# Kernel optimization log

Measured on AMD Instinct MI355X. Metric: run time of the kernel, lower is better.

The kernel has to match this reference:

```python
import jax, jax.numpy as jnp
import numpy as np

N = 20000      # nodes
E = 320000     # edges
B = 128        # graphs in batch
DIN = 64       # in_channels == out_channels (residual)
DEDGE = 64     # edge_attr_dim
DINS = 64      # ins_dim
H = 2          # heads
C = 64         # out_channels per head
L = 2          # num_ins (conv layers)
SLOPE = 0.2    # leaky relu negative slope
EPS = 1e-5     # batchnorm eps


def setup_inputs() -> dict:
    key = jax.random.key(0)
    ks = jax.random.split(key, 12)
    s = 0.05  # small glorot-ish init scale
    return {
        "x": jax.random.normal(ks[0], (N, DIN), jnp.float32),
        "edge_index": jax.random.randint(ks[1], (2, E), 0, N),
        "edge_attr": jax.random.normal(ks[2], (E, DEDGE), jnp.float32),
        "instr_vectors": jax.random.normal(ks[3], (L, B, DINS), jnp.float32),
        "batch": jnp.sort(jax.random.randint(ks[4], (N,), 0, B)),
        "W_l": jax.random.normal(ks[5], (L, DIN + DINS, H * C), jnp.float32) * s,
        "W_e": jax.random.normal(ks[6], (L, DEDGE + DINS, H * C), jnp.float32) * s,
        "att_l": jax.random.normal(ks[7], (L, H, C), jnp.float32) * s,
        "att_r": jax.random.normal(ks[8], (L, H, C), jnp.float32) * s,
        "att_e": jax.random.normal(ks[9], (L, H, C), jnp.float32) * s,
        "bias": jnp.zeros((L, C), jnp.float32),
        "bn_gamma": jnp.ones((L - 1, C), jnp.float32),
        "bn_beta": jnp.zeros((L - 1, C), jnp.float32),
    }


def reference(x, edge_index, edge_attr, instr_vectors, batch,
              W_l, W_e, att_l, att_r, att_e, bias, bn_gamma, bn_beta):
    src, dst = edge_index[0], edge_index[1]  # j -> i (source_to_target)
    h = x
    for i in range(L):
        ins = instr_vectors[i]                                   # [B, DINS]
        x_cat = jnp.concatenate([h, ins[batch]], axis=-1)        # [N, DIN+DINS]
        e_cat = jnp.concatenate([edge_attr, ins[batch[src]]], axis=-1)  # [E, ...]
        xl = (x_cat @ W_l[i]).reshape(-1, H, C)                  # [N,H,C] (lin_l == lin_r)
        al = (xl * att_l[i]).sum(-1)                             # [N,H]
        ar = (xl * att_r[i]).sum(-1)                             # [N,H]
        eh = (e_cat @ W_e[i]).reshape(-1, H, C)                  # [E,H,C]
        ae = (eh * att_e[i]).sum(-1)                             # [E,H]
        a = al[src] + ar[dst] + ae                               # [E,H]
        a = jnp.where(a > 0, a, SLOPE * a)                       # leaky relu
        # segment softmax over incoming edges of each target node
        m = jax.ops.segment_max(a, dst, num_segments=N)          # [N,H]
        ex = jnp.exp(a - m[dst])
        ssum = jax.ops.segment_sum(ex, dst, num_segments=N)
        alpha = ex / (ssum[dst] + 1e-16)                         # [E,H]
        out = jax.ops.segment_sum(xl[src] * alpha[:, :, None], dst, num_segments=N)
        out = out.mean(axis=1) + bias[i]                         # concat=False -> head mean
        h = out + h                                              # residual
        if i != L - 1:
            mu = h.mean(axis=0)
            var = ((h - mu) ** 2).mean(axis=0)                   # biased var (BN training)
            h = (h - mu) / jnp.sqrt(var + EPS) * bn_gamma[i] + bn_beta[i]
            h = jax.nn.relu(h)
    return h
```

## Files before the change

### kernel.cpp

```cpp
#include <hip/hip_runtime.h>
#include <hip/hip_fp16.h>
#include <math.h>

#define NN 20000
#define NE 320000
#define NB 128
#define SLOPE 0.2f
#define BN_EPS 1e-5f
#define ROWS 65
#define PBKT 256

__device__ __forceinline__ unsigned short f2bf(float f) {
    unsigned int u = __float_as_uint(f);
    unsigned int r = (u + 0x7FFFu + ((u >> 16) & 1u)) >> 16;
    return (unsigned short)r;
}
__device__ __forceinline__ float bf2f(unsigned short h) {
    return __uint_as_float(((unsigned int)h) << 16);
}

__global__ __launch_bounds__(256) void k_front(const int* __restrict__ dst, int* __restrict__ deg,
                                               const float* __restrict__ instr, const float* __restrict__ Wl,
                                               const float* __restrict__ We, const float* __restrict__ atte,
                                               float* __restrict__ insl01, float* __restrict__ ve01,
                                               float* __restrict__ ce01) {
    __shared__ float w2[128];
    int blk = blockIdx.x, t = threadIdx.x;
    if (blk < 1250) {
        int e = blk * 256 + t;
        atomicAdd(&deg[dst[e]], 1);
    } else if (blk < 1378) {
        int bb = blk - 1250;
        int L = bb >> 6;
        int idx = (bb & 63) * 256 + t;
        int b = idx >> 7, j = idx & 127;
        const float* ins = instr + (size_t)L * NB * 64;
        const float* WlL = Wl + (size_t)L * 128 * 128;
        float acc = 0.f;
        for (int k = 0; k < 64; ++k) acc += ins[b * 64 + k] * WlL[(64 + k) * 128 + j];
        insl01[(size_t)L * 16384 + idx] = acc;
    } else {
        int L = blk - 1378;
        const float* WeL = We + (size_t)L * 128 * 128;
        const float* aeL = atte + L * 128;
        int h = (t >> 6) & 1;
        int k = t & 63;
        int row = (t < 128) ? k : (64 + k);
        float acc = 0.f;
        for (int c = 0; c < 64; ++c) acc += WeL[row * 128 + h * 64 + c] * aeL[h * 64 + c];
        if (t < 128) ve01[L * 128 + t] = acc;
        else        w2[t - 128] = acc;
        __syncthreads();
        int b = t >> 1, hh = t & 1;
        const float* ins = instr + (size_t)L * NB * 64;
        float a2 = 0.f;
        for (int kk = 0; kk < 64; ++kk) a2 += ins[b * 64 + kk] * w2[hh * 64 + kk];
        ce01[L * 256 + b * 2 + hh] = a2;
    }
}

__global__ __launch_bounds__(1024) void k_scan(const int* __restrict__ deg,
                                               int* __restrict__ rowptr, int* __restrict__ cursor) {
    __shared__ int wsum[16];
    int t = threadIdx.x, lane = t & 63, w = t >> 6;
    int running = 0;
    for (int r = 0; r < 20; ++r) {
        int idx = r * 1024 + t;
        int v = (idx < NN) ? deg[idx] : 0;
        int incl = v;
        for (int off = 1; off < 64; off <<= 1) { int u = __shfl_up(incl, off); if (lane >= off) incl += u; }
        if (lane == 63) wsum[w] = incl;
        __syncthreads();
        int pre = 0, tot = 0;
        for (int i = 0; i < 16; ++i) { int s = wsum[i]; tot += s; if (i < w) pre += s; }
        int excl = running + pre + incl - v;
        if (idx < NN) { rowptr[idx] = excl; cursor[idx] = excl; }
        running += tot;
        __syncthreads();
    }
    if (t == 0) rowptr[NN] = running;
}

__global__ __launch_bounds__(256) void k_node(const float* __restrict__ hcur, const float* __restrict__ Wl,
                                              const float* __restrict__ insl, const int* __restrict__ batch,
                                              const float* __restrict__ attl, const float* __restrict__ attr_,
                                              const float2* __restrict__ ce2,
                                              const float* __restrict__ scsh, int use_bn,
                                              unsigned short* __restrict__ xlh,
                                              float* __restrict__ alc, float* __restrict__ ar) {
    __shared__ float sh[8 * 64];
    int t = threadIdx.x;
    int row0 = blockIdx.x * 8;
    for (int idx = t; idx < 512; idx += 256) {
        int r = idx >> 6, k = idx & 63;
        int n = row0 + r;
        float hv = (n < NN) ? hcur[n * 64 + k] : 0.f;
        if (use_bn) hv = fmaxf(hv * scsh[k] + scsh[64 + k], 0.f);
        sh[idx] = hv;
    }
    __syncthreads();
    int w = t >> 6, lane = t & 63;
    int h = w & 1;
    int rbase = (w >> 1) * 4;
    int j = h * 64 + lane;
    float attlv = attl[j];
    float attrv = attr_[j];
    float acc0 = 0.f, acc1 = 0.f, acc2 = 0.f, acc3 = 0.f;
    for (int k = 0; k < 64; ++k) {
        float wv = Wl[k * 128 + j];
        acc0 += sh[(rbase + 0) * 64 + k] * wv;
        acc1 += sh[(rbase + 1) * 64 + k] * wv;
        acc2 += sh[(rbase + 2) * 64 + k] * wv;
        acc3 += sh[(rbase + 3) * 64 + k] * wv;
    }
    float accs[4] = {acc0, acc1, acc2, acc3};
    for (int rr = 0; rr < 4; ++rr) {
        int n = row0 + rbase + rr;
        if (n >= NN) break;
        int b = batch[n];
        float v = accs[rr] + insl[b * 128 + j];
        xlh[(size_t)n * 128 + j] = f2bf(v);
        float pl = v * attlv, pr = v * attrv;
        for (int off = 32; off > 0; off >>= 1) {
            pl += __shfl_xor(pl, off);
            pr += __shfl_xor(pr, off);
        }
        if (lane == 0) {
            float2 cb = ce2[b];
            alc[n * 2 + h] = pl + (h ? cb.y : cb.x);
            ar[n * 2 + h] = pr;
        }
    }
}

__global__ __launch_bounds__(64) void k_sced(const int* __restrict__ src, const int* __restrict__ dst,
                                             const float* __restrict__ eattr, const float* __restrict__ ve01,
                                             const float2* __restrict__ alc2, const float2* __restrict__ ar2,
                                             int* __restrict__ cursor, int4* __restrict__ einfo) {
    __shared__ float se[64 * ROWS];
    __shared__ float svT[256];
    int lane = threadIdx.x;
#pragma unroll
    for (int i = 0; i < 4; ++i) {
        int idx = i * 64 + lane;
        svT[idx] = ve01[(idx & 3) * 64 + (idx >> 2)];
    }
    int ebase = blockIdx.x * 64;
    const float4* gsrc = (const float4*)eattr + (size_t)ebase * 16;
#pragma unroll
    for (int i = 0; i < 16; ++i) {
        int fi = i * 64 + lane;
        float4 f = gsrc[fi];
        int el = fi >> 4, q = fi & 15;
        float* dp = se + el * ROWS + q * 4;
        dp[0] = f.x; dp[1] = f.y; dp[2] = f.z; dp[3] = f.w;
    }
    const float* row = se + lane * ROWS;
    float d0 = 0.f, d1 = 0.f, d2 = 0.f, d3 = 0.f;
#pragma unroll
    for (int k = 0; k < 64; ++k) {
        float fv = row[k];
        float4 vt = *(const float4*)&svT[4 * k];
        d0 += fv * vt.x; d1 += fv * vt.y; d2 += fv * vt.z; d3 += fv * vt.w;
    }
    int e = ebase + lane;
    int s = src[e], dd = dst[e];
    float2 al = alc2[s], arr = ar2[dd];
    float a0 = al.x + arr.x + d0;
    float a1 = al.y + arr.y + d1;
    a0 = (a0 > 0.f) ? a0 : SLOPE * a0;
    a1 = (a1 > 0.f) ? a1 : SLOPE * a1;
    __half2 ex = __floats2half2_rn(__expf(a0), __expf(a1));
    __half2 d23 = __floats2half2_rn(d2, d3);
    int pos = atomicAdd(&cursor[dd], 1);
    einfo[pos] = make_int4(s | (dd << 15), *(int*)&d23, s, *(int*)&ex);
}

__global__ __launch_bounds__(256) void k_gather0(const int* __restrict__ rowptr, const int2* __restrict__ rec,
                                                 const unsigned int* __restrict__ xl32,
                                                 const float* __restrict__ bias, const float* __restrict__ hprev,
                                                 float* __restrict__ hnew, float* __restrict__ part) {
    __shared__ float smv[4][64];
    __shared__ float smq[4][64];
    int t = threadIdx.x;
    int w = t >> 6, lane = t & 63;
    int n = blockIdx.x * 4 + w;
    int r0 = rowptr[n], r1 = rowptr[n + 1];
    float acc0 = 0.f, acc1 = 0.f, ss = 0.f;
    const unsigned int* xlp = xl32 + lane;
#pragma unroll 8
    for (int p = r0; p < r1; ++p) {
        int2 r = rec[(size_t)p * 2];
        __half2 hx = *(__half2*)&r.y;
        float2 e2 = __half22float2(hx);
        float ex = (lane < 32) ? e2.x : e2.y;
        unsigned int pr = xlp[(size_t)r.x * 64];
        ss += ex;
        acc0 += ex * bf2f((unsigned short)(pr & 0xFFFFu));
        acc1 += ex * bf2f((unsigned short)(pr >> 16));
    }
    float inv_s = 1.f / (ss + 1e-16f);
    acc0 *= inv_s; acc1 *= inv_s;
    float o0 = 0.5f * (acc0 + __shfl_xor(acc0, 32));
    float o1 = 0.5f * (acc1 + __shfl_xor(acc1, 32));
    if (lane < 32) {
        float2 hv = ((const float2*)(hprev + (size_t)n * 64))[lane];
        float2 bv = ((const float2*)bias)[lane];
        float2 o;
        o.x = o0 + bv.x + hv.x;
        o.y = o1 + bv.y + hv.y;
        ((float2*)(hnew + (size_t)n * 64))[lane] = o;
        smv[w][2 * lane]     = o.x;
        smv[w][2 * lane + 1] = o.y;
        smq[w][2 * lane]     = o.x * o.x;
        smq[w][2 * lane + 1] = o.y * o.y;
    }
    __syncthreads();
    if (t < 128) {
        int c = t & 63, which = t >> 6;
        float a = which ? (smq[0][c] + smq[1][c] + smq[2][c] + smq[3][c])
                        : (smv[0][c] + smv[1][c] + smv[2][c] + smv[3][c]);
        atomicAdd(&part[(blockIdx.x & (PBKT - 1)) * 128 + which * 64 + c], a);
    }
}

__global__ __launch_bounds__(512) void k_bnfin(const float* __restrict__ part,
                                               const float* __restrict__ gamma, const float* __restrict__ beta,
                                               float* __restrict__ scsh) {
    __shared__ float red[512];
    __shared__ float tot[128];
    int t = threadIdx.x;
    int col = t & 127, q = t >> 7;
    float s = 0.f;
    for (int r = q * (PBKT / 4); r < (q + 1) * (PBKT / 4); ++r) s += part[r * 128 + col];
    red[t] = s;
    __syncthreads();
    if (t < 128) tot[t] = red[t] + red[t + 128] + red[t + 256] + red[t + 384];
    __syncthreads();
    if (t < 64) {
        float su = tot[t];
        float sq = tot[64 + t];
        float mu = su * (1.f / NN);
        float var = sq * (1.f / NN) - mu * mu;
        float sc = gamma[t] * rsqrtf(var + BN_EPS);
        scsh[t] = sc;
        scsh[64 + t] = beta[t] - mu * sc;
    }
}

__global__ __launch_bounds__(256) void k_gather1(const int* __restrict__ rowptr, const int4* __restrict__ einfo,
                                                 const float2* __restrict__ alc2, const float2* __restrict__ ar2,
                                                 const unsigned int* __restrict__ xl32,
                                                 const float* __restrict__ bias, const float* __restrict__ hprev,
                                                 const float* __restrict__ scsh, float* __restrict__ out) {
    int t = threadIdx.x;
    int w = t >> 6, lane = t & 63;
    int n = blockIdx.x * 4 + w;
    int r0 = rowptr[n], r1 = rowptr[n + 1];
    float2 arr = ar2[n];
    float acc0 = 0.f, acc1 = 0.f, ss = 0.f;
    const unsigned int* xlp = xl32 + lane;
#pragma unroll 4
    for (int p = r0; p < r1; ++p) {
        int4 r = einfo[p];
        int s = r.z;
        float2 dv = __half22float2(*(__half2*)&r.y);
        float2 al = alc2[s];
        float a0 = al.x + arr.x + dv.x;
        float a1 = al.y + arr.y + dv.y;
        a0 = (a0 > 0.f) ? a0 : SLOPE * a0;
        a1 = (a1 > 0.f) ? a1 : SLOPE * a1;
        float e0 = __expf(a0), e1 = __expf(a1);
        float ex = (lane < 32) ? e0 : e1;
        unsigned int pr = xlp[(size_t)s * 64];
        ss += ex;
        acc0 += ex * bf2f((unsigned short)(pr & 0xFFFFu));
        acc1 += ex * bf2f((unsigned short)(pr >> 16));
    }
    float inv_s = 1.f / (ss + 1e-16f);
    acc0 *= inv_s; acc1 *= inv_s;
    float o0 = 0.5f * (acc0 + __shfl_xor(acc0, 32));
    float o1 = 0.5f * (acc1 + __shfl_xor(acc1, 32));
    if (lane < 32) {
        float2 hv = ((const float2*)(hprev + (size_t)n * 64))[lane];
        float2 sc = ((const float2*)scsh)[lane];
        float2 sf = ((const float2*)(scsh + 64))[lane];
        hv.x = fmaxf(hv.x * sc.x + sf.x, 0.f);
        hv.y = fmaxf(hv.y * sc.y + sf.y, 0.f);
        float2 bv = ((const float2*)bias)[lane];
        float2 o;
        o.x = o0 + bv.x + hv.x;
        o.y = o1 + bv.y + hv.y;
        ((float2*)(out + (size_t)n * 64))[lane] = o;
    }
}

extern "C" void kernel_launch(void* const* d_in, const int* in_sizes, int n_in,
                              void* d_out, int out_size, void* d_ws, size_t ws_size,
                              hipStream_t stream) {
    (void)in_sizes; (void)n_in; (void)out_size; (void)ws_size;
    const float* x     = (const float*)d_in[0];
    const int*   eidx  = (const int*)d_in[1];
    const float* eattr = (const float*)d_in[2];
    const float* instr = (const float*)d_in[3];
    const int*   batch = (const int*)d_in[4];
    const float* W_l   = (const float*)d_in[5];
    const float* W_e   = (const float*)d_in[6];
    const float* att_l = (const float*)d_in[7];
    const float* att_r = (const float*)d_in[8];
    const float* att_e = (const float*)d_in[9];
    const float* bias  = (const float*)d_in[10];
    const float* bn_g  = (const float*)d_in[11];
    const float* bn_b  = (const float*)d_in[12];
    float* out = (float*)d_out;

    const int* src = eidx;
    const int* dst = eidx + NE;

    char* ws = (char*)d_ws;
    int4*   einfo   = (int4*)ws;       ws += (size_t)NE * 16;
    unsigned short* xlh = (unsigned short*)ws; ws += (size_t)NN * 128 * 2;
    int*    deg     = (int*)ws;        ws += NN * 4;
    float*  part    = (float*)ws;      ws += PBKT * 128 * 4;
    int*    rowptr  = (int*)ws;        ws += (NN + 1) * 4 + 12;
    int*    cursor  = (int*)ws;        ws += NN * 4;
    float*  alc     = (float*)ws;      ws += NN * 2 * 4;
    float*  ar      = (float*)ws;      ws += NN * 2 * 4;
    float*  insl01  = (float*)ws;      ws += 2 * 128 * 128 * 4;
    float*  ve01    = (float*)ws;      ws += 256 * 4;
    float*  ce01    = (float*)ws;      ws += 2 * 256 * 4;
    float*  hbuf    = (float*)ws;      ws += (size_t)NN * 64 * 4;
    float*  scsh    = (float*)ws;      ws += 128 * 4;

    hipMemsetAsync(deg, 0, NN * 4 + PBKT * 128 * 4, stream);

    k_front<<<1380, 256, 0, stream>>>(dst, deg, instr, W_l, W_e, att_e, insl01, ve01, ce01);
    k_scan<<<1, 1024, 0, stream>>>(deg, rowptr, cursor);
    k_node<<<(NN + 7) / 8, 256, 0, stream>>>(x, W_l, insl01, batch,
                                             att_l, att_r, (const float2*)ce01,
                                             scsh, 0, xlh, alc, ar);
    k_sced<<<NE / 64, 64, 0, stream>>>(src, dst, eattr, ve01,
                                       (const float2*)alc, (const float2*)ar, cursor, einfo);
    k_gather0<<<NN / 4, 256, 0, stream>>>(rowptr, (const int2*)einfo + 1,
                                          (const unsigned int*)xlh, bias, x, hbuf, part);
    k_bnfin<<<1, 512, 0, stream>>>(part, bn_g, bn_b, scsh);
    k_node<<<(NN + 7) / 8, 256, 0, stream>>>(hbuf, W_l + 128 * 128, insl01 + 16384, batch,
                                             att_l + 128, att_r + 128, (const float2*)(ce01 + 256),
                                             scsh, 1, xlh, alc, ar);
    k_gather1<<<NN / 4, 256, 0, stream>>>(rowptr, einfo, (const float2*)alc, (const float2*)ar,
                                          (const unsigned int*)xlh, bias + 64, hbuf, scsh, out);
}
```

Before: 311.7 us.

## Parallelize degree scan, split layer-2 attention exp into edge-parallel kernel, halve sced LDS

Replaces the single-block serial prefix scan with a three-kernel multi-block scan (block sums, block offsets, local scan). Moves layer-2 attention logit, leaky-relu and exp computation out of the per-node gather loop into a separate edge-parallel kernel that writes compact (src, half2 exp) records, so the gather streams 8-byte records instead of 16-byte ones and does no transcendental work. The edge score kernel now stages edge attributes in two halves to use half the shared memory, which may raise occupancy. The cost is two extra kernel launches plus an extra pass over the edge records.

New measurement: 288.7 us. -7.4%, faster.

```diff
diff --git a/kernel.cpp b/kernel.cpp
--- a/kernel.cpp
+++ b/kernel.cpp
@@ -7,8 +7,9 @@
 #define NB 128
 #define SLOPE 0.2f
 #define BN_EPS 1e-5f
-#define ROWS 65
+#define NBLK 79
 #define PBKT 256
+#define ROWS_H 33
 
 __device__ __forceinline__ unsigned short f2bf(float f) {
     unsigned int u = __float_as_uint(f);
@@ -59,26 +60,46 @@
     }
 }
 
-__global__ __launch_bounds__(1024) void k_scan(const int* __restrict__ deg,
+__global__ __launch_bounds__(256) void k_scanA(const int* __restrict__ deg, int* __restrict__ bsum) {
+    __shared__ int wsum[4];
+    int t = threadIdx.x;
+    int idx = blockIdx.x * 256 + t;
+    int v = (idx < NN) ? deg[idx] : 0;
+    for (int off = 32; off > 0; off >>= 1) v += __shfl_xor(v, off);
+    if ((t & 63) == 0) wsum[t >> 6] = v;
+    __syncthreads();
+    if (t == 0) bsum[blockIdx.x] = wsum[0] + wsum[1] + wsum[2] + wsum[3];
+}
+
+__global__ __launch_bounds__(64) void k_scanB(const int* __restrict__ bsum, int* __restrict__ boff,
+                                              int* __restrict__ rowptr) {
+    int l = threadIdx.x;
+    int v0 = (l < NBLK) ? bsum[l] : 0;
+    int v1 = (64 + l < NBLK) ? bsum[64 + l] : 0;
+    int o0 = v0, o1 = v1;
+    for (int off = 1; off < 64; off <<= 1) { int u = __shfl_up(v0, off); if (l >= off) v0 += u; }
+    int tot0 = __shfl(v0, 63);
+    for (int off = 1; off < 64; off <<= 1) { int u = __shfl_up(v1, off); if (l >= off) v1 += u; }
+    int tot1 = __shfl(v1, 63);
+    if (l < NBLK) boff[l] = v0 - o0;
+    if (64 + l < NBLK) boff[64 + l] = tot0 + v1 - o1;
+    if (l == 0) rowptr[NN] = tot0 + tot1;
+}
+
+__global__ __launch_bounds__(256) void k_scanC(const int* __restrict__ deg, const int* __restrict__ boff,
                                                int* __restrict__ rowptr, int* __restrict__ cursor) {
-    __shared__ int wsum[16];
+    __shared__ int wsum[4];
     int t = threadIdx.x, lane = t & 63, w = t >> 6;
-    int running = 0;
-    for (int r = 0; r < 20; ++r) {
-        int idx = r * 1024 + t;
-        int v = (idx < NN) ? deg[idx] : 0;
-        int incl = v;
-        for (int off = 1; off < 64; off <<= 1) { int u = __shfl_up(incl, off); if (lane >= off) incl += u; }
-        if (lane == 63) wsum[w] = incl;
-        __syncthreads();
-        int pre = 0, tot = 0;
-        for (int i = 0; i < 16; ++i) { int s = wsum[i]; tot += s; if (i < w) pre += s; }
-        int excl = running + pre + incl - v;
-        if (idx < NN) { rowptr[idx] = excl; cursor[idx] = excl; }
-        running += tot;
-        __syncthreads();
-    }
-    if (t == 0) rowptr[NN] = running;
+    int idx = blockIdx.x * 256 + t;
+    int v = (idx < NN) ? deg[idx] : 0;
+    int incl = v;
+    for (int off = 1; off < 64; off <<= 1) { int u = __shfl_up(incl, off); if (lane >= off) incl += u; }
+    if (lane == 63) wsum[w] = incl;
+    __syncthreads();
+    int pre = 0;
+    for (int i = 0; i < w; ++i) pre += wsum[i];
+    int excl = incl - v + pre + boff[blockIdx.x];
+    if (idx < NN) { rowptr[idx] = excl; cursor[idx] = excl; }
 }
 
 __global__ __launch_bounds__(256) void k_node(const float* __restrict__ hcur, const float* __restrict__ Wl,
@@ -137,7 +158,7 @@
                                              const float* __restrict__ eattr, const float* __restrict__ ve01,
                                              const float2* __restrict__ alc2, const float2* __restrict__ ar2,
                                              int* __restrict__ cursor, int4* __restrict__ einfo) {
-    __shared__ float se[64 * ROWS];
+    __shared__ float se[64 * ROWS_H];
     __shared__ float svT[256];
     int lane = threadIdx.x;
 #pragma unroll
@@ -146,22 +167,26 @@
         svT[idx] = ve01[(idx & 3) * 64 + (idx >> 2)];
     }
     int ebase = blockIdx.x * 64;
-    const float4* gsrc = (const float4*)eattr + (size_t)ebase * 16;
+    float d0 = 0.f, d1 = 0.f, d2 = 0.f, d3 = 0.f;
+    const float* row = se + lane * ROWS_H;
 #pragma unroll
-    for (int i = 0; i < 16; ++i) {
-        int fi = i * 64 + lane;
-        float4 f = gsrc[fi];
-        int el = fi >> 4, q = fi & 15;
-        float* dp = se + el * ROWS + q * 4;
-        dp[0] = f.x; dp[1] = f.y; dp[2] = f.z; dp[3] = f.w;
-    }
-    const float* row = se + lane * ROWS;
-    float d0 = 0.f, d1 = 0.f, d2 = 0.f, d3 = 0.f;
+    for (int half = 0; half < 2; ++half) {
+        const float4* gsrc = (const float4*)eattr + (size_t)ebase * 16 + half * 8;
 #pragma unroll
-    for (int k = 0; k < 64; ++k) {
-        float fv = row[k];
-        float4 vt = *(const float4*)&svT[4 * k];
-        d0 += fv * vt.x; d1 += fv * vt.y; d2 += fv * vt.z; d3 += fv * vt.w;
+        for (int i = 0; i < 8; ++i) {
+            int fi = i * 64 + lane;
+            int el = fi >> 3, q = fi & 7;
+            float4 f = gsrc[(size_t)el * 16 + q];
+            float* dp = se + el * ROWS_H + q * 4;
+            dp[0] = f.x; dp[1] = f.y; dp[2] = f.z; dp[3] = f.w;
+        }
+        const float* vbase = svT + half * 128;
+#pragma unroll
+        for (int k = 0; k < 32; ++k) {
+            float fv = row[k];
+            float4 vt = *(const float4*)&vbase[4 * k];
+            d0 += fv * vt.x; d1 += fv * vt.y; d2 += fv * vt.z; d3 += fv * vt.w;
+        }
     }
     int e = ebase + lane;
     int s = src[e], dd = dst[e];
@@ -248,8 +273,26 @@
     }
 }
 
-__global__ __launch_bounds__(256) void k_gather1(const int* __restrict__ rowptr, const int4* __restrict__ einfo,
+__global__ __launch_bounds__(256) void k_attnexp(const int4* __restrict__ einfo,
                                                  const float2* __restrict__ alc2, const float2* __restrict__ ar2,
+                                                 int2* __restrict__ rec1) {
+    int p = blockIdx.x * 256 + threadIdx.x;
+    if (p >= NE) return;
+    int4 r = einfo[p];
+    int s = r.x & 0x7FFF, d = r.x >> 15;
+    __half2 hd = *(__half2*)&r.y;
+    float2 dv = __half22float2(hd);
+    float2 a_l = alc2[s];
+    float2 a_r = ar2[d];
+    float a0 = a_l.x + a_r.x + dv.x;
+    float a1 = a_l.y + a_r.y + dv.y;
+    a0 = (a0 > 0.f) ? a0 : SLOPE * a0;
+    a1 = (a1 > 0.f) ? a1 : SLOPE * a1;
+    __half2 hx = __floats2half2_rn(__expf(a0), __expf(a1));
+    rec1[p] = make_int2(s, *(int*)&hx);
+}
+
+__global__ __launch_bounds__(256) void k_gather1(const int* __restrict__ rowptr, const int2* __restrict__ rec,
                                                  const unsigned int* __restrict__ xl32,
                                                  const float* __restrict__ bias, const float* __restrict__ hprev,
                                                  const float* __restrict__ scsh, float* __restrict__ out) {
@@ -257,22 +300,15 @@
     int w = t >> 6, lane = t & 63;
     int n = blockIdx.x * 4 + w;
     int r0 = rowptr[n], r1 = rowptr[n + 1];
-    float2 arr = ar2[n];
     float acc0 = 0.f, acc1 = 0.f, ss = 0.f;
     const unsigned int* xlp = xl32 + lane;
-#pragma unroll 4
+#pragma unroll 8
     for (int p = r0; p < r1; ++p) {
-        int4 r = einfo[p];
-        int s = r.z;
-        float2 dv = __half22float2(*(__half2*)&r.y);
-        float2 al = alc2[s];
-        float a0 = al.x + arr.x + dv.x;
-        float a1 = al.y + arr.y + dv.y;
-        a0 = (a0 > 0.f) ? a0 : SLOPE * a0;
-        a1 = (a1 > 0.f) ? a1 : SLOPE * a1;
-        float e0 = __expf(a0), e1 = __expf(a1);
-        float ex = (lane < 32) ? e0 : e1;
-        unsigned int pr = xlp[(size_t)s * 64];
+        int2 r = rec[p];
+        __half2 hx = *(__half2*)&r.y;
+        float2 e2 = __half22float2(hx);
+        float ex = (lane < 32) ? e2.x : e2.y;
+        unsigned int pr = xlp[(size_t)r.x * 64];
         ss += ex;
         acc0 += ex * bf2f((unsigned short)(pr & 0xFFFFu));
         acc1 += ex * bf2f((unsigned short)(pr >> 16));
@@ -319,11 +355,14 @@
 
     char* ws = (char*)d_ws;
     int4*   einfo   = (int4*)ws;       ws += (size_t)NE * 16;
+    int2*   rec1    = (int2*)ws;       ws += (size_t)NE * 8;
     unsigned short* xlh = (unsigned short*)ws; ws += (size_t)NN * 128 * 2;
     int*    deg     = (int*)ws;        ws += NN * 4;
     float*  part    = (float*)ws;      ws += PBKT * 128 * 4;
     int*    rowptr  = (int*)ws;        ws += (NN + 1) * 4 + 12;
     int*    cursor  = (int*)ws;        ws += NN * 4;
+    int*    bsum    = (int*)ws;        ws += 80 * 4;
+    int*    boff    = (int*)ws;        ws += 80 * 4;
     float*  alc     = (float*)ws;      ws += NN * 2 * 4;
     float*  ar      = (float*)ws;      ws += NN * 2 * 4;
     float*  insl01  = (float*)ws;      ws += 2 * 128 * 128 * 4;
@@ -335,7 +374,9 @@
     hipMemsetAsync(deg, 0, NN * 4 + PBKT * 128 * 4, stream);
 
     k_front<<<1380, 256, 0, stream>>>(dst, deg, instr, W_l, W_e, att_e, insl01, ve01, ce01);
-    k_scan<<<1, 1024, 0, stream>>>(deg, rowptr, cursor);
+    k_scanA<<<NBLK, 256, 0, stream>>>(deg, bsum);
+    k_scanB<<<1, 64, 0, stream>>>(bsum, boff, rowptr);
+    k_scanC<<<NBLK, 256, 0, stream>>>(deg, boff, rowptr, cursor);
     k_node<<<(NN + 7) / 8, 256, 0, stream>>>(x, W_l, insl01, batch,
                                              att_l, att_r, (const float2*)ce01,
                                              scsh, 0, xlh, alc, ar);
@@ -347,6 +388,7 @@
     k_node<<<(NN + 7) / 8, 256, 0, stream>>>(hbuf, W_l + 128 * 128, insl01 + 16384, batch,
                                              att_l + 128, att_r + 128, (const float2*)(ce01 + 256),
                                              scsh, 1, xlh, alc, ar);
-    k_gather1<<<NN / 4, 256, 0, stream>>>(rowptr, einfo, (const float2*)alc, (const float2*)ar,
-                                          (const unsigned int*)xlh, bias + 64, hbuf, scsh, out);
-}
+    k_attnexp<<<(NE + 255) / 256, 256, 0, stream>>>(einfo, (const float2*)alc, (const float2*)ar, rec1);
+    k_gather1<<<NN / 4, 256, 0, stream>>>(rowptr, rec1, (const unsigned int*)xlh,
+                                          bias + 64, hbuf, scsh, out);
+}
```
